# Performance work log

Hardware: AMD Instinct MI355X
Metric: run time of the kernel (lower is better)

## Reference

```python
import jax, jax.numpy as jnp
import numpy as np

# norse LIFParameters defaults
ALPHA = 100.0        # superspike surrogate slope
DT = 1e-3
TAU_SYN_INV = 200.0  # 1/5e-3
TAU_MEM_INV = 100.0  # 1/1e-2
V_TH = 1.0           # v_leak = v_reset = 0

@jax.custom_vjp
def heaviside(v):
    # forward: hard threshold; backward: superspike surrogate 1/(alpha*|v|+1)^2
    return (v > 0).astype(v.dtype)

def _hv_fwd(v):
    return heaviside(v), v

def _hv_bwd(v, g):
    return (g / (ALPHA * jnp.abs(v) + 1.0) ** 2,)

heaviside.defvjp(_hv_fwd, _hv_bwd)

def setup_inputs() -> dict:
    key = jax.random.key(0)
    ks = jax.random.split(key, 5)
    B, H, W, O = 2048, 15, 15, 10
    x = jax.random.uniform(ks[0], (B, 1, H, W), jnp.float32)  # image-like in [0,1)
    conv_w = jax.random.normal(ks[1], (2, 1, 4, 4), jnp.float32) * 0.25
    conv_b = jax.random.normal(ks[2], (2,), jnp.float32) * 0.1
    lin_w = jax.random.normal(ks[3], (O, 72), jnp.float32) * (1.0 / np.sqrt(72.0))
    lin_b = jax.random.normal(ks[4], (O,), jnp.float32) * 0.1
    return {"x": x, "conv_w": conv_w, "conv_b": conv_b,
            "lin_w": lin_w, "lin_b": lin_b, "num_steps": 300}

def reference(x, conv_w, conv_b, lin_w, lin_b, num_steps):
    B = x.shape[0]
    O = lin_w.shape[0]
    current = x * 10.0  # constant input current to the encoder

    def step(carry, _):
        v_enc, v, i = carry
        # --- constant_current_lif_encode step (lif_current_encoder) ---
        v_enc = v_enc + DT * TAU_MEM_INV * (-v_enc + current)
        z_in = heaviside(v_enc - V_TH)
        v_enc = v_enc - z_in * v_enc  # reset to v_reset = 0
        # --- feed-forward: conv -> maxpool(2) -> linear ---
        c = jax.lax.conv_general_dilated(
            z_in, conv_w, (1, 1), 'VALID',
            dimension_numbers=('NCHW', 'OIHW', 'NCHW')) + conv_b[None, :, None, None]
        p = jax.lax.reduce_window(c, -jnp.inf, jax.lax.max,
                                  (1, 1, 2, 2), (1, 1, 2, 2), 'VALID')  # [B,2,6,6]
        lin = p.reshape(B, -1) @ lin_w.T + lin_b  # [B,O]
        # --- norse LIFCell (lif_feed_forward_step) ---
        v_dec = v + DT * TAU_MEM_INV * (-v + i)
        i_dec = i - DT * TAU_SYN_INV * i
        spk = heaviside(v_dec - V_TH)
        v_new = (1.0 - spk) * v_dec  # v_reset = 0
        i_new = i_dec + lin
        return (v_enc, v_new, i_new), (spk, v_new)

    init = (jnp.zeros_like(current),
            jnp.zeros((B, O), x.dtype),
            jnp.zeros((B, O), x.dtype))
    _, (spk_rec, mem_rec) = jax.lax.scan(step, init, None, length=num_steps)
    spk_out = spk_rec.sum(0)  # [B,O]
    return spk_out, mem_rec, spk_rec
```

## Files before the change

### kernel.cpp

```cpp
#include <hip/hip_runtime.h>
#include <math.h>


typedef float v2f __attribute__((ext_vector_type(2)));

__global__ __launch_bounds__(128, 4) void snn_step_kernel(
    const float* __restrict__ x,
    const float* __restrict__ conv_w,
    const float* __restrict__ conv_b,
    const float* __restrict__ lin_w,
    const float* __restrict__ lin_b,
    float* __restrict__ out,
    int T, int B)
{
    const int b   = blockIdx.x;
    const int tid = threadIdx.x;
    const int w   = tid & 63;
    const int wv  = tid >> 6;

    __shared__ float  s_linw[720];
    __shared__ float  s_linb[10];
    __shared__ float4 s_lut[4][32];
    __shared__ unsigned int s_bits[2][16];
    __shared__ float  s_p[8][72];
    __shared__ float  s_part[64];

    for (int j = tid; j < 720; j += 128) s_linw[j] = lin_w[j];
    if (tid < 10) s_linb[tid] = lin_b[tid];
    {
        const int ky = tid >> 5, n = tid & 31;
        float s00 = 0.f, s01 = 0.f, s10 = 0.f, s11 = 0.f;
#pragma unroll
        for (int kx = 0; kx < 4; ++kx) {
            const float w0 = conv_w[ky * 4 + kx];
            const float w1 = conv_w[16 + ky * 4 + kx];
            if ((n >> kx) & 1)       { s00 += w0; s01 += w1; }
            if ((n >> (kx + 1)) & 1) { s10 += w0; s11 += w1; }
        }
        s_lut[ky][n] = make_float4(s00, s01, s10, s11);
    }
    __syncthreads();

    float ve[4], cur[4];
    v2f  cb2 = (v2f){0.f, 0.f};
    bool convlane = false;
    int  wordsel = 0, shx = 0, shx16 = 16;

    float lwreg[18];
    float lbias = 0.f;
    float v = 0.f, i_syn = 0.f, sc = 0.f;
    float svv[4], svs[4];
    const int lo = w >> 2, lq = w & 3;
    const size_t BO = (size_t)B * 10;
    float* mp  = out + BO + (size_t)b * 10 + w;
    float* spp = out + BO + (size_t)T * BO + (size_t)b * 10 + w;

    auto enc_pack = [&](int bufsel) {
        unsigned long long bal0, bal1, bal2, bal3;
        {
            float vn = __fadd_rn(ve[0], __fmul_rn(0.1f, __fsub_rn(cur[0], ve[0])));
            bool  sp = (vn > 1.0f);
            ve[0] = sp ? 0.f : vn;
            bal0  = __ballot(sp);
        }
        {
            float vn = __fadd_rn(ve[1], __fmul_rn(0.1f, __fsub_rn(cur[1], ve[1])));
            bool  sp = (vn > 1.0f);
            ve[1] = sp ? 0.f : vn;
            bal1  = __ballot(sp);
        }
        {
            float vn = __fadd_rn(ve[2], __fmul_rn(0.1f, __fsub_rn(cur[2], ve[2])));
            bool  sp = (vn > 1.0f);
            ve[2] = sp ? 0.f : vn;
            bal2  = __ballot(sp);
        }
        {
            float vn = __fadd_rn(ve[3], __fmul_rn(0.1f, __fsub_rn(cur[3], ve[3])));
            bool  sp = (vn > 1.0f);
            ve[3] = sp ? 0.f : vn;
            bal3  = __ballot(sp);
        }
        unsigned long long m01 = (w & 2) ? bal1 : bal0;
        unsigned long long m23 = (w & 2) ? bal3 : bal2;
        unsigned long long m   = (w & 4) ? m23 : m01;
        unsigned word = (unsigned)((w & 1) ? (m >> 32) : m);
        if (w < 8) s_bits[bufsel][w] = word;
    };

    if (wv == 0) {
        const int j   = w >> 4;
        const int col = w & 15;
#pragma unroll
        for (int k = 0; k < 4; ++k) {
            const int  row = 4 * k + j;
            const bool act = (col < 15) && (row < 15);
            ve[k]  = 0.f;
            cur[k] = act ? __fmul_rn(x[(size_t)b * 225 + row * 15 + col], 10.0f) : 0.f;
        }
        convlane = (w < 36);
        const int py = w / 6, px = w - 6 * py;
        wordsel = py;
        shx     = 2 * px;
        shx16   = shx + 16;
        cb2 = (v2f){conv_b[0], conv_b[1]};

        enc_pack(0);
    } else {
#pragma unroll
        for (int jj = 0; jj < 18; ++jj) {
            int idx = lo * 72 + lq * 18 + jj;
            lwreg[jj] = s_linw[idx < 720 ? idx : 719];
        }
        lbias = (w < 10) ? s_linb[w] : 0.f;
    }

    auto lin_comp = [&](const float* pbuf, int k) {
        const float* pp = &pbuf[lq * 18];
        float pv[18];
#pragma unroll
        for (int jj = 0; jj < 18; ++jj) pv[jj] = pp[jj];
        float partial = 0.0f;
#pragma unroll
        for (int jj = 0; jj < 18; ++jj)
            partial = fmaf(lwreg[jj], pv[jj], partial);
        s_part[w] = partial;

        float vd  = __fadd_rn(v, __fmul_rn(0.1f, __fsub_rn(i_syn, v)));
        float id  = __fsub_rn(i_syn, __fmul_rn(0.2f, i_syn));
        float spk = (vd > 1.0f) ? 1.0f : 0.0f;
        v = (vd > 1.0f) ? 0.0f : vd;
        sc += spk;
        svv[k] = v;
        svs[k] = spk;

        float4 pr = *(const float4*)&s_part[4 * (w < 10 ? w : 0)];
        float lin = __fadd_rn(__fadd_rn(__fadd_rn(__fadd_rn(pr.x, pr.y), pr.z), pr.w), lbias);
        i_syn = __fadd_rn(id, lin);
    };

    auto issue_stores = [&]() {
        if (w < 10) {
#pragma unroll
            for (int k = 0; k < 4; ++k) {
                mp[(size_t)k * BO]  = svv[k];
                spp[(size_t)k * BO] = svs[k];
            }
        }
        mp  += 4 * BO;
        spp += 4 * BO;
    };

    const int TI = T >> 2;

    for (int i = 0; i < TI; ++i) {
        if (wv == 0) {
#pragma unroll
            for (int k = 0; k < 4; ++k) {
                unsigned wb0 = 0, wb1 = 0, wb2 = 0;
                if (convlane) {
                    const unsigned* bb = &s_bits[k & 1][wordsel];
                    wb0 = bb[0]; wb1 = bb[1]; wb2 = bb[2];
                }

                enc_pack((k + 1) & 1);

                if (convlane) {
                    const int i0 = (wb0 >> shx)   & 31;
                    const int i1 = (wb0 >> shx16) & 31;
                    const int i2 = (wb1 >> shx)   & 31;
                    const int i3 = (wb1 >> shx16) & 31;
                    const int i4 = (wb2 >> shx)   & 31;

                    const float4 f0 = s_lut[0][i0];
                    const float4 f1 = s_lut[1][i1];
                    const float4 f2 = s_lut[2][i2];
                    const float4 f3 = s_lut[3][i3];
                    const float4 g0 = s_lut[0][i1];
                    const float4 g1 = s_lut[1][i2];
                    const float4 g2 = s_lut[2][i3];
                    const float4 g3 = s_lut[3][i4];

                    v2f a00 = (v2f){f0.x, f0.y};  a00 += (v2f){f1.x, f1.y};
                    a00 += (v2f){f2.x, f2.y};     a00 += (v2f){f3.x, f3.y};
                    v2f a01 = (v2f){f0.z, f0.w};  a01 += (v2f){f1.z, f1.w};
                    a01 += (v2f){f2.z, f2.w};     a01 += (v2f){f3.z, f3.w};
                    v2f a10 = (v2f){g0.x, g0.y};  a10 += (v2f){g1.x, g1.y};
                    a10 += (v2f){g2.x, g2.y};     a10 += (v2f){g3.x, g3.y};
                    v2f a11 = (v2f){g0.z, g0.w};  a11 += (v2f){g1.z, g1.w};
                    a11 += (v2f){g2.z, g2.w};     a11 += (v2f){g3.z, g3.w};

                    v2f v00 = a00 + cb2, v01 = a01 + cb2;
                    v2f v10 = a10 + cb2, v11 = a11 + cb2;
                    v2f m2 = __builtin_elementwise_max(
                                 __builtin_elementwise_max(v00, v01),
                                 __builtin_elementwise_max(v10, v11));

                    float* pbuf = s_p[((i & 1) << 2) | k];
                    pbuf[w]      = m2.x;
                    pbuf[36 + w] = m2.y;
                }
            }
        } else {
            if (i >= 2) issue_stores();
            if (i >= 1) {
#pragma unroll
                for (int k = 0; k < 4; ++k)
                    lin_comp(s_p[(((i - 1) & 1) << 2) | k], k);
            }
        }
        __syncthreads();
    }

    if (wv == 1) {
        issue_stores();
#pragma unroll
        for (int k = 0; k < 4; ++k)
            lin_comp(s_p[(((TI - 1) & 1) << 2) | k], k);
        issue_stores();
        if (w < 10) out[(size_t)b * 10 + w] = sc;
    }
}

extern "C" void kernel_launch(void* const* d_in, const int* in_sizes, int n_in,
                              void* d_out, int out_size, void* d_ws, size_t ws_size,
                              hipStream_t stream) {
    const float* x      = (const float*)d_in[0];
    const float* conv_w = (const float*)d_in[1];
    const float* conv_b = (const float*)d_in[2];
    const float* lin_w  = (const float*)d_in[3];
    const float* lin_b  = (const float*)d_in[4];
    float* out = (float*)d_out;

    const int B = in_sizes[0] / 225;
    const int T = (out_size / (B * 10) - 1) / 2;

    snn_step_kernel<<<B, 128, 0, stream>>>(x, conv_w, conv_b, lin_w, lin_b, out, T, B);
}
```

Before: 203.9 us.

## Merge producer and consumer waves into a single barrier-free wave

Collapses the two-wave block (encoder/conv wave and linear/LIF wave synchronized by __syncthreads) into one 64-lane wave that software-pipelines encode, conv and linear/LIF across consecutive timesteps. The pooled-feature buffer is repacked with padding so each quarter starts at a 20-float offset, and outputs are stored every step. This removes block barriers and cross-wave handoff, and halves threads per block so more blocks can be resident. In exchange the wave serializes all stage work and relies on intra-wave lockstep for shared-memory ordering.

```diff
diff --git a/kernel.cpp b/kernel.cpp
--- a/kernel.cpp
+++ b/kernel.cpp
@@ -4,7 +4,7 @@
 
 typedef float v2f __attribute__((ext_vector_type(2)));
 
-__global__ __launch_bounds__(128, 4) void snn_step_kernel(
+__global__ __launch_bounds__(64, 2) void snn_step_kernel(
     const float* __restrict__ x,
     const float* __restrict__ conv_w,
     const float* __restrict__ conv_b,
@@ -13,22 +13,22 @@
     float* __restrict__ out,
     int T, int B)
 {
-    const int b   = blockIdx.x;
-    const int tid = threadIdx.x;
-    const int w   = tid & 63;
-    const int wv  = tid >> 6;
+    const int b = blockIdx.x;
+    const int w = threadIdx.x;
 
     __shared__ float  s_linw[720];
     __shared__ float  s_linb[10];
     __shared__ float4 s_lut[4][32];
     __shared__ unsigned int s_bits[2][16];
-    __shared__ float  s_p[8][72];
+    __shared__ float  s_p[2][80];
     __shared__ float  s_part[64];
 
-    for (int j = tid; j < 720; j += 128) s_linw[j] = lin_w[j];
-    if (tid < 10) s_linb[tid] = lin_b[tid];
-    {
-        const int ky = tid >> 5, n = tid & 31;
+    for (int j = w; j < 720; j += 64) s_linw[j] = lin_w[j];
+    if (w < 10) s_linb[w] = lin_b[w];
+#pragma unroll
+    for (int e = 0; e < 2; ++e) {
+        const int t  = w + 64 * e;
+        const int ky = t >> 5, n = t & 31;
         float s00 = 0.f, s01 = 0.f, s10 = 0.f, s11 = 0.f;
 #pragma unroll
         for (int kx = 0; kx < 4; ++kx) {
@@ -41,16 +41,32 @@
     }
     __syncthreads();
 
+    const int jrow = w >> 4, col = w & 15;
     float ve[4], cur[4];
-    v2f  cb2 = (v2f){0.f, 0.f};
-    bool convlane = false;
-    int  wordsel = 0, shx = 0, shx16 = 16;
-
+#pragma unroll
+    for (int k = 0; k < 4; ++k) {
+        const int  row = 4 * k + jrow;
+        const bool act = (col < 15) && (row < 15);
+        ve[k]  = 0.f;
+        cur[k] = act ? __fmul_rn(x[(size_t)b * 225 + row * 15 + col], 10.0f) : 0.f;
+    }
+
+    const bool convlane = (w < 36);
+    const int py = w / 6, px = w - 6 * py;
+    const int wordsel = py;
+    const int shx = 2 * px, shx16 = shx + 16;
+    const int off0 = (w < 18) ? w : (w + 2);
+    const v2f cb2 = (v2f){conv_b[0], conv_b[1]};
+
+    const int lo = w >> 2, lq = w & 3;
     float lwreg[18];
-    float lbias = 0.f;
+#pragma unroll
+    for (int jj = 0; jj < 18; ++jj) {
+        int idx = lo * 72 + lq * 18 + jj;
+        lwreg[jj] = s_linw[idx < 720 ? idx : 719];
+    }
+    const float lbias = (w < 10) ? s_linb[w] : 0.f;
     float v = 0.f, i_syn = 0.f, sc = 0.f;
-    float svv[4], svs[4];
-    const int lo = w >> 2, lq = w & 3;
     const size_t BO = (size_t)B * 10;
     float* mp  = out + BO + (size_t)b * 10 + w;
     float* spp = out + BO + (size_t)T * BO + (size_t)b * 10 + w;
@@ -88,38 +104,74 @@
         if (w < 8) s_bits[bufsel][w] = word;
     };
 
-    if (wv == 0) {
-        const int j   = w >> 4;
-        const int col = w & 15;
-#pragma unroll
-        for (int k = 0; k < 4; ++k) {
-            const int  row = 4 * k + j;
-            const bool act = (col < 15) && (row < 15);
-            ve[k]  = 0.f;
-            cur[k] = act ? __fmul_rn(x[(size_t)b * 225 + row * 15 + col], 10.0f) : 0.f;
-        }
-        convlane = (w < 36);
-        const int py = w / 6, px = w - 6 * py;
-        wordsel = py;
-        shx     = 2 * px;
-        shx16   = shx + 16;
-        cb2 = (v2f){conv_b[0], conv_b[1]};
-
-        enc_pack(0);
-    } else {
-#pragma unroll
-        for (int jj = 0; jj < 18; ++jj) {
-            int idx = lo * 72 + lq * 18 + jj;
-            lwreg[jj] = s_linw[idx < 720 ? idx : 719];
-        }
-        lbias = (w < 10) ? s_linb[w] : 0.f;
-    }
-
-    auto lin_comp = [&](const float* pbuf, int k) {
-        const float* pp = &pbuf[lq * 18];
+    auto conv_lut = [&](unsigned wb0, unsigned wb1, unsigned wb2, int dbuf) {
+        const int i0 = (wb0 >> shx)   & 31;
+        const int i1 = (wb0 >> shx16) & 31;
+        const int i2 = (wb1 >> shx)   & 31;
+        const int i3 = (wb1 >> shx16) & 31;
+        const int i4 = (wb2 >> shx)   & 31;
+
+        const float4 f0 = s_lut[0][i0];
+        const float4 f1 = s_lut[1][i1];
+        const float4 f2 = s_lut[2][i2];
+        const float4 f3 = s_lut[3][i3];
+        const float4 g0 = s_lut[0][i1];
+        const float4 g1 = s_lut[1][i2];
+        const float4 g2 = s_lut[2][i3];
+        const float4 g3 = s_lut[3][i4];
+
+        v2f a00 = (v2f){f0.x, f0.y};  a00 += (v2f){f1.x, f1.y};
+        a00 += (v2f){f2.x, f2.y};     a00 += (v2f){f3.x, f3.y};
+        v2f a01 = (v2f){f0.z, f0.w};  a01 += (v2f){f1.z, f1.w};
+        a01 += (v2f){f2.z, f2.w};     a01 += (v2f){f3.z, f3.w};
+        v2f a10 = (v2f){g0.x, g0.y};  a10 += (v2f){g1.x, g1.y};
+        a10 += (v2f){g2.x, g2.y};     a10 += (v2f){g3.x, g3.y};
+        v2f a11 = (v2f){g0.z, g0.w};  a11 += (v2f){g1.z, g1.w};
+        a11 += (v2f){g2.z, g2.w};     a11 += (v2f){g3.z, g3.w};
+
+        v2f v00 = a00 + cb2, v01 = a01 + cb2;
+        v2f v10 = a10 + cb2, v11 = a11 + cb2;
+        v2f m2 = __builtin_elementwise_max(
+                     __builtin_elementwise_max(v00, v01),
+                     __builtin_elementwise_max(v10, v11));
+
+        float* pbuf = s_p[dbuf];
+        pbuf[off0]      = m2.x;
+        pbuf[off0 + 40] = m2.y;
+    };
+
+    enc_pack(0);
+    enc_pack(1);
+    {
+        unsigned wb0 = 0, wb1 = 0, wb2 = 0;
+        if (convlane) {
+            const unsigned* bb = &s_bits[0][wordsel];
+            wb0 = bb[0]; wb1 = bb[1]; wb2 = bb[2];
+        }
+        if (convlane) conv_lut(wb0, wb1, wb2, 0);
+    }
+
+    for (int i = 0; i < T; ++i) {
+        const int pb = i & 1;
+        const int cb = pb ^ 1;
+
+        unsigned wb0 = 0, wb1 = 0, wb2 = 0;
+        if (convlane) {
+            const unsigned* bb = &s_bits[cb][wordsel];
+            wb0 = bb[0]; wb1 = bb[1]; wb2 = bb[2];
+        }
+
         float pv[18];
-#pragma unroll
-        for (int jj = 0; jj < 18; ++jj) pv[jj] = pp[jj];
+        {
+            const float* pp = &s_p[pb][lq * 20];
+#pragma unroll
+            for (int jj = 0; jj < 18; ++jj) pv[jj] = pp[jj];
+        }
+
+        enc_pack(pb);
+
+        if (convlane) conv_lut(wb0, wb1, wb2, cb);
+
         float partial = 0.0f;
 #pragma unroll
         for (int jj = 0; jj < 18; ++jj)
@@ -131,95 +183,17 @@
         float spk = (vd > 1.0f) ? 1.0f : 0.0f;
         v = (vd > 1.0f) ? 0.0f : vd;
         sc += spk;
-        svv[k] = v;
-        svs[k] = spk;
 
         float4 pr = *(const float4*)&s_part[4 * (w < 10 ? w : 0)];
         float lin = __fadd_rn(__fadd_rn(__fadd_rn(__fadd_rn(pr.x, pr.y), pr.z), pr.w), lbias);
         i_syn = __fadd_rn(id, lin);
-    };
-
-    auto issue_stores = [&]() {
-        if (w < 10) {
-#pragma unroll
-            for (int k = 0; k < 4; ++k) {
-                mp[(size_t)k * BO]  = svv[k];
-                spp[(size_t)k * BO] = svs[k];
-            }
-        }
-        mp  += 4 * BO;
-        spp += 4 * BO;
-    };
-
-    const int TI = T >> 2;
-
-    for (int i = 0; i < TI; ++i) {
-        if (wv == 0) {
-#pragma unroll
-            for (int k = 0; k < 4; ++k) {
-                unsigned wb0 = 0, wb1 = 0, wb2 = 0;
-                if (convlane) {
-                    const unsigned* bb = &s_bits[k & 1][wordsel];
-                    wb0 = bb[0]; wb1 = bb[1]; wb2 = bb[2];
-                }
-
-                enc_pack((k + 1) & 1);
-
-                if (convlane) {
-                    const int i0 = (wb0 >> shx)   & 31;
-                    const int i1 = (wb0 >> shx16) & 31;
-                    const int i2 = (wb1 >> shx)   & 31;
-                    const int i3 = (wb1 >> shx16) & 31;
-                    const int i4 = (wb2 >> shx)   & 31;
-
-                    const float4 f0 = s_lut[0][i0];
-                    const float4 f1 = s_lut[1][i1];
-                    const float4 f2 = s_lut[2][i2];
-                    const float4 f3 = s_lut[3][i3];
-                    const float4 g0 = s_lut[0][i1];
-                    const float4 g1 = s_lut[1][i2];
-                    const float4 g2 = s_lut[2][i3];
-                    const float4 g3 = s_lut[3][i4];
-
-                    v2f a00 = (v2f){f0.x, f0.y};  a00 += (v2f){f1.x, f1.y};
-                    a00 += (v2f){f2.x, f2.y};     a00 += (v2f){f3.x, f3.y};
-                    v2f a01 = (v2f){f0.z, f0.w};  a01 += (v2f){f1.z, f1.w};
-                    a01 += (v2f){f2.z, f2.w};     a01 += (v2f){f3.z, f3.w};
-                    v2f a10 = (v2f){g0.x, g0.y};  a10 += (v2f){g1.x, g1.y};
-                    a10 += (v2f){g2.x, g2.y};     a10 += (v2f){g3.x, g3.y};
-                    v2f a11 = (v2f){g0.z, g0.w};  a11 += (v2f){g1.z, g1.w};
-                    a11 += (v2f){g2.z, g2.w};     a11 += (v2f){g3.z, g3.w};
-
-                    v2f v00 = a00 + cb2, v01 = a01 + cb2;
-                    v2f v10 = a10 + cb2, v11 = a11 + cb2;
-                    v2f m2 = __builtin_elementwise_max(
-                                 __builtin_elementwise_max(v00, v01),
-                                 __builtin_elementwise_max(v10, v11));
-
-                    float* pbuf = s_p[((i & 1) << 2) | k];
-                    pbuf[w]      = m2.x;
-                    pbuf[36 + w] = m2.y;
-                }
-            }
-        } else {
-            if (i >= 2) issue_stores();
-            if (i >= 1) {
-#pragma unroll
-                for (int k = 0; k < 4; ++k)
-                    lin_comp(s_p[(((i - 1) & 1) << 2) | k], k);
-            }
-        }
-        __syncthreads();
-    }
-
-    if (wv == 1) {
-        issue_stores();
-#pragma unroll
-        for (int k = 0; k < 4; ++k)
-            lin_comp(s_p[(((TI - 1) & 1) << 2) | k], k);
-        issue_stores();
-        if (w < 10) out[(size_t)b * 10 + w] = sc;
-    }
+
+        if (w < 10) { *mp = v; *spp = spk; }
+        mp  += BO;
+        spp += BO;
+    }
+
+    if (w < 10) out[(size_t)b * 10 + w] = sc;
 }
 
 extern "C" void kernel_launch(void* const* d_in, const int* in_sizes, int n_in,
@@ -235,5 +209,5 @@
     const int B = in_sizes[0] / 225;
     const int T = (out_size / (B * 10) - 1) / 2;
 
-    snn_step_kernel<<<B, 128, 0, stream>>>(x, conv_w, conv_b, lin_w, lin_b, out, T, B);
+    snn_step_kernel<<<B, 64, 0, stream>>>(x, conv_w, conv_b, lin_w, lin_b, out, T, B);
 }
```

After: 212.7 us. +4.3%, slower.

## Split pipeline across three waves: encoder/decoder wave and two conv+linear waves

Applied to the files above, without the earlier changes.

Moves from a two-wave pipeline to three waves per block. One wave handles encoding and the LIF decode, and two waves share the conv+pool+linear work by alternating timesteps. An 8-slot spike-bit ring and a per-step linear-result buffer let these stages run in parallel. The role-to-wave mapping is rotated per block, presumably to spread load across SIMDs. This shortens the critical per-group work but raises threads per block and the number of pipeline stages, which lengthens prologue and epilogue and may lower occupancy.

```diff
diff --git a/kernel.cpp b/kernel.cpp
--- a/kernel.cpp
+++ b/kernel.cpp
@@ -4,7 +4,7 @@
 
 typedef float v2f __attribute__((ext_vector_type(2)));
 
-__global__ __launch_bounds__(128, 4) void snn_step_kernel(
+__global__ __launch_bounds__(192, 6) void snn_step_kernel(
     const float* __restrict__ x,
     const float* __restrict__ conv_w,
     const float* __restrict__ conv_b,
@@ -13,21 +13,23 @@
     float* __restrict__ out,
     int T, int B)
 {
-    const int b   = blockIdx.x;
-    const int tid = threadIdx.x;
-    const int w   = tid & 63;
-    const int wv  = tid >> 6;
-
-    __shared__ float  s_linw[720];
-    __shared__ float  s_linb[10];
-    __shared__ float4 s_lut[4][32];
-    __shared__ unsigned int s_bits[2][16];
-    __shared__ float  s_p[8][72];
-    __shared__ float  s_part[64];
-
-    for (int j = tid; j < 720; j += 128) s_linw[j] = lin_w[j];
+    const int b    = blockIdx.x;
+    const int tid  = threadIdx.x;
+    const int w    = tid & 63;
+    const int wv   = tid >> 6;
+    const int role = (wv + b) % 3;
+
+    __shared__ float    s_linw[720];
+    __shared__ float    s_linb[10];
+    __shared__ float4   s_lut[4][32];
+    __shared__ unsigned s_bits[8][16];
+    __shared__ float    s_lin[8][12];
+    __shared__ float    s_p[2][80];
+    __shared__ float    s_part[2][64];
+
+    for (int j = tid; j < 720; j += 192) s_linw[j] = lin_w[j];
     if (tid < 10) s_linb[tid] = lin_b[tid];
-    {
+    if (tid < 128) {
         const int ky = tid >> 5, n = tid & 31;
         float s00 = 0.f, s01 = 0.f, s10 = 0.f, s11 = 0.f;
 #pragma unroll
@@ -42,20 +44,39 @@
     __syncthreads();
 
     float ve[4], cur[4];
-    v2f  cb2 = (v2f){0.f, 0.f};
-    bool convlane = false;
-    int  wordsel = 0, shx = 0, shx16 = 16;
-
-    float lwreg[18];
-    float lbias = 0.f;
     float v = 0.f, i_syn = 0.f, sc = 0.f;
     float svv[4], svs[4];
-    const int lo = w >> 2, lq = w & 3;
     const size_t BO = (size_t)B * 10;
     float* mp  = out + BO + (size_t)b * 10 + w;
     float* spp = out + BO + (size_t)T * BO + (size_t)b * 10 + w;
-
-    auto enc_pack = [&](int bufsel) {
+    {
+        const int jrow = w >> 4, col = w & 15;
+#pragma unroll
+        for (int k = 0; k < 4; ++k) {
+            const int  row = 4 * k + jrow;
+            const bool act = (col < 15) && (row < 15) && (role == 0);
+            ve[k]  = 0.f;
+            cur[k] = act ? __fmul_rn(x[(size_t)b * 225 + row * 15 + col], 10.0f) : 0.f;
+        }
+    }
+
+    const int  r1 = (role == 2) ? 1 : 0;
+    const bool convlane = (w < 36);
+    const int  py = w / 6, px = w - 6 * py;
+    const int  wordsel = py;
+    const int  shx = 2 * px, shx16 = shx + 16;
+    const int  off0 = (w < 18) ? w : (w + 2);
+    const v2f  cb2 = (v2f){conv_b[0], conv_b[1]};
+    const int  lo = w >> 2, lq = w & 3;
+    float lwreg[18];
+#pragma unroll
+    for (int jj = 0; jj < 18; ++jj) {
+        int idx = lo * 72 + lq * 18 + jj;
+        lwreg[jj] = s_linw[idx < 720 ? idx : 719];
+    }
+    const float lbias = (w < 10) ? s_linb[w] : 0.f;
+
+    auto enc_pack = [&](int slot) {
         unsigned long long bal0, bal1, bal2, bal3;
         {
             float vn = __fadd_rn(ve[0], __fmul_rn(0.1f, __fsub_rn(cur[0], ve[0])));
@@ -85,47 +106,72 @@
         unsigned long long m23 = (w & 2) ? bal3 : bal2;
         unsigned long long m   = (w & 4) ? m23 : m01;
         unsigned word = (unsigned)((w & 1) ? (m >> 32) : m);
-        if (w < 8) s_bits[bufsel][w] = word;
-    };
-
-    if (wv == 0) {
-        const int j   = w >> 4;
-        const int col = w & 15;
-#pragma unroll
-        for (int k = 0; k < 4; ++k) {
-            const int  row = 4 * k + j;
-            const bool act = (col < 15) && (row < 15);
-            ve[k]  = 0.f;
-            cur[k] = act ? __fmul_rn(x[(size_t)b * 225 + row * 15 + col], 10.0f) : 0.f;
-        }
-        convlane = (w < 36);
-        const int py = w / 6, px = w - 6 * py;
-        wordsel = py;
-        shx     = 2 * px;
-        shx16   = shx + 16;
-        cb2 = (v2f){conv_b[0], conv_b[1]};
-
-        enc_pack(0);
-    } else {
-#pragma unroll
-        for (int jj = 0; jj < 18; ++jj) {
-            int idx = lo * 72 + lq * 18 + jj;
-            lwreg[jj] = s_linw[idx < 720 ? idx : 719];
-        }
-        lbias = (w < 10) ? s_linb[w] : 0.f;
-    }
-
-    auto lin_comp = [&](const float* pbuf, int k) {
-        const float* pp = &pbuf[lq * 18];
+        if (w < 8) s_bits[slot][w] = word;
+    };
+
+    auto conv_lin = [&](int t) {
+        const int slot = t & 7;
+        if (convlane) {
+            const unsigned* bb = &s_bits[slot][wordsel];
+            const unsigned wb0 = bb[0], wb1 = bb[1], wb2 = bb[2];
+
+            const int i0 = (wb0 >> shx)   & 31;
+            const int i1 = (wb0 >> shx16) & 31;
+            const int i2 = (wb1 >> shx)   & 31;
+            const int i3 = (wb1 >> shx16) & 31;
+            const int i4 = (wb2 >> shx)   & 31;
+
+            const float4 f0 = s_lut[0][i0];
+            const float4 f1 = s_lut[1][i1];
+            const float4 f2 = s_lut[2][i2];
+            const float4 f3 = s_lut[3][i3];
+            const float4 g0 = s_lut[0][i1];
+            const float4 g1 = s_lut[1][i2];
+            const float4 g2 = s_lut[2][i3];
+            const float4 g3 = s_lut[3][i4];
+
+            v2f a00 = (v2f){f0.x, f0.y};  a00 += (v2f){f1.x, f1.y};
+            a00 += (v2f){f2.x, f2.y};     a00 += (v2f){f3.x, f3.y};
+            v2f a01 = (v2f){f0.z, f0.w};  a01 += (v2f){f1.z, f1.w};
+            a01 += (v2f){f2.z, f2.w};     a01 += (v2f){f3.z, f3.w};
+            v2f a10 = (v2f){g0.x, g0.y};  a10 += (v2f){g1.x, g1.y};
+            a10 += (v2f){g2.x, g2.y};     a10 += (v2f){g3.x, g3.y};
+            v2f a11 = (v2f){g0.z, g0.w};  a11 += (v2f){g1.z, g1.w};
+            a11 += (v2f){g2.z, g2.w};     a11 += (v2f){g3.z, g3.w};
+
+            v2f v00 = a00 + cb2, v01 = a01 + cb2;
+            v2f v10 = a10 + cb2, v11 = a11 + cb2;
+            v2f m2 = __builtin_elementwise_max(
+                         __builtin_elementwise_max(v00, v01),
+                         __builtin_elementwise_max(v10, v11));
+
+            float* pbuf = s_p[r1];
+            pbuf[off0]      = m2.x;
+            pbuf[off0 + 40] = m2.y;
+        }
+        asm volatile("" ::: "memory");
+
         float pv[18];
-#pragma unroll
-        for (int jj = 0; jj < 18; ++jj) pv[jj] = pp[jj];
+        {
+            const float* pp = &s_p[r1][lq * 20];
+#pragma unroll
+            for (int jj = 0; jj < 18; ++jj) pv[jj] = pp[jj];
+        }
         float partial = 0.0f;
 #pragma unroll
         for (int jj = 0; jj < 18; ++jj)
             partial = fmaf(lwreg[jj], pv[jj], partial);
-        s_part[w] = partial;
-
+        s_part[r1][w] = partial;
+        asm volatile("" ::: "memory");
+
+        float4 pr = *(const float4*)&s_part[r1][4 * (w < 10 ? w : 0)];
+        float lin = __fadd_rn(__fadd_rn(__fadd_rn(__fadd_rn(pr.x, pr.y), pr.z), pr.w), lbias);
+        if (w < 10) s_lin[slot][w] = lin;
+    };
+
+    const int li = (w < 10) ? w : 10;
+    auto dec_step = [&](int t, int k) {
+        float lv  = s_lin[t & 7][li];
         float vd  = __fadd_rn(v, __fmul_rn(0.1f, __fsub_rn(i_syn, v)));
         float id  = __fsub_rn(i_syn, __fmul_rn(0.2f, i_syn));
         float spk = (vd > 1.0f) ? 1.0f : 0.0f;
@@ -133,10 +179,7 @@
         sc += spk;
         svv[k] = v;
         svs[k] = spk;
-
-        float4 pr = *(const float4*)&s_part[4 * (w < 10 ? w : 0)];
-        float lin = __fadd_rn(__fadd_rn(__fadd_rn(__fadd_rn(pr.x, pr.y), pr.z), pr.w), lbias);
-        i_syn = __fadd_rn(id, lin);
+        i_syn = __fadd_rn(id, lv);
     };
 
     auto issue_stores = [&]() {
@@ -151,72 +194,44 @@
         spp += 4 * BO;
     };
 
-    const int TI = T >> 2;
-
-    for (int i = 0; i < TI; ++i) {
-        if (wv == 0) {
-#pragma unroll
-            for (int k = 0; k < 4; ++k) {
-                unsigned wb0 = 0, wb1 = 0, wb2 = 0;
-                if (convlane) {
-                    const unsigned* bb = &s_bits[k & 1][wordsel];
-                    wb0 = bb[0]; wb1 = bb[1]; wb2 = bb[2];
-                }
-
-                enc_pack((k + 1) & 1);
-
-                if (convlane) {
-                    const int i0 = (wb0 >> shx)   & 31;
-                    const int i1 = (wb0 >> shx16) & 31;
-                    const int i2 = (wb1 >> shx)   & 31;
-                    const int i3 = (wb1 >> shx16) & 31;
-                    const int i4 = (wb2 >> shx)   & 31;
-
-                    const float4 f0 = s_lut[0][i0];
-                    const float4 f1 = s_lut[1][i1];
-                    const float4 f2 = s_lut[2][i2];
-                    const float4 f3 = s_lut[3][i3];
-                    const float4 g0 = s_lut[0][i1];
-                    const float4 g1 = s_lut[1][i2];
-                    const float4 g2 = s_lut[2][i3];
-                    const float4 g3 = s_lut[3][i4];
-
-                    v2f a00 = (v2f){f0.x, f0.y};  a00 += (v2f){f1.x, f1.y};
-                    a00 += (v2f){f2.x, f2.y};     a00 += (v2f){f3.x, f3.y};
-                    v2f a01 = (v2f){f0.z, f0.w};  a01 += (v2f){f1.z, f1.w};
-                    a01 += (v2f){f2.z, f2.w};     a01 += (v2f){f3.z, f3.w};
-                    v2f a10 = (v2f){g0.x, g0.y};  a10 += (v2f){g1.x, g1.y};
-                    a10 += (v2f){g2.x, g2.y};     a10 += (v2f){g3.x, g3.y};
-                    v2f a11 = (v2f){g0.z, g0.w};  a11 += (v2f){g1.z, g1.w};
-                    a11 += (v2f){g2.z, g2.w};     a11 += (v2f){g3.z, g3.w};
-
-                    v2f v00 = a00 + cb2, v01 = a01 + cb2;
-                    v2f v10 = a10 + cb2, v11 = a11 + cb2;
-                    v2f m2 = __builtin_elementwise_max(
-                                 __builtin_elementwise_max(v00, v01),
-                                 __builtin_elementwise_max(v10, v11));
-
-                    float* pbuf = s_p[((i & 1) << 2) | k];
-                    pbuf[w]      = m2.x;
-                    pbuf[36 + w] = m2.y;
-                }
+    const int NG = T >> 2;
+
+    for (int g = 0; g < NG; ++g) {
+        const int base = 4 * g;
+        if (role == 0) {
+            if (g >= 3) issue_stores();
+#pragma unroll
+            for (int k = 0; k < 4; ++k)
+                enc_pack((base + k) & 7);
+            if (g >= 2) {
+#pragma unroll
+                for (int k = 0; k < 4; ++k)
+                    dec_step(base - 8 + k, k);
             }
         } else {
-            if (i >= 2) issue_stores();
-            if (i >= 1) {
-#pragma unroll
-                for (int k = 0; k < 4; ++k)
-                    lin_comp(s_p[(((i - 1) & 1) << 2) | k], k);
+            if (g >= 1) {
+                for (int k = role - 1; k < 4; k += 2)
+                    conv_lin(base - 4 + k);
             }
         }
         __syncthreads();
     }
 
-    if (wv == 1) {
+    if (role != 0) {
+        for (int k = role - 1; k < 4; k += 2)
+            conv_lin(T - 4 + k);
+    } else {
         issue_stores();
 #pragma unroll
         for (int k = 0; k < 4; ++k)
-            lin_comp(s_p[(((TI - 1) & 1) << 2) | k], k);
+            dec_step(T - 8 + k, k);
+    }
+    __syncthreads();
+    if (role == 0) {
+        issue_stores();
+#pragma unroll
+        for (int k = 0; k < 4; ++k)
+            dec_step(T - 4 + k, k);
         issue_stores();
         if (w < 10) out[(size_t)b * 10 + w] = sc;
     }
@@ -235,5 +250,5 @@
     const int B = in_sizes[0] / 225;
     const int T = (out_size / (B * 10) - 1) / 2;
 
-    snn_step_kernel<<<B, 128, 0, stream>>>(x, conv_w, conv_b, lin_w, lin_b, out, T, B);
+    snn_step_kernel<<<B, 192, 0, stream>>>(x, conv_w, conv_b, lin_w, lin_b, out, T, B);
 }
```

Measured after the change: 256.7 us. +25.9%, slower.

## Rebalance warp pipeline: 6-step groups, split conv across waves, shuffle reductions

Applied to the files above, without the earlier changes.

Each barrier interval now covers 6 timesteps instead of 4, and the spike bitmasks and pooled buffers become 16-slot rings. Wave 0 encodes 6 steps and convolves 4 of them, while wave 1 convolves the remaining 2 before running the linear and LIF updates. The linear partial-sum reduction uses xor shuffles in place of an LDS round trip, which removes the s_part scratch buffer. The aim is to balance work between the two waves and reduce barriers per step, at the cost of more LDS and registers and an assumption that T is divisible by 6.

```diff
diff --git a/kernel.cpp b/kernel.cpp
--- a/kernel.cpp
+++ b/kernel.cpp
@@ -18,12 +18,11 @@
     const int w   = tid & 63;
     const int wv  = tid >> 6;
 
-    __shared__ float  s_linw[720];
-    __shared__ float  s_linb[10];
-    __shared__ float4 s_lut[4][32];
-    __shared__ unsigned int s_bits[2][16];
-    __shared__ float  s_p[8][72];
-    __shared__ float  s_part[64];
+    __shared__ float    s_linw[720];
+    __shared__ float    s_linb[10];
+    __shared__ float4   s_lut[4][32];
+    __shared__ unsigned s_bits[16][8];
+    __shared__ float    s_p[16][80];
 
     for (int j = tid; j < 720; j += 128) s_linw[j] = lin_w[j];
     if (tid < 10) s_linb[tid] = lin_b[tid];
@@ -42,20 +41,39 @@
     __syncthreads();
 
     float ve[4], cur[4];
-    v2f  cb2 = (v2f){0.f, 0.f};
-    bool convlane = false;
-    int  wordsel = 0, shx = 0, shx16 = 16;
-
+    {
+        const int jrow = w >> 4, col = w & 15;
+#pragma unroll
+        for (int k = 0; k < 4; ++k) {
+            const int  row = 4 * k + jrow;
+            const bool act = (col < 15) && (row < 15) && (wv == 0);
+            ve[k]  = 0.f;
+            cur[k] = act ? __fmul_rn(x[(size_t)b * 225 + row * 15 + col], 10.0f) : 0.f;
+        }
+    }
+
+    const bool convlane = (w < 36);
+    const int  py = w / 6, px = w - 6 * py;
+    const int  wordsel = py;
+    const int  shx = 2 * px, shx16 = shx + 16;
+    const int  off0 = (w < 18) ? w : (w + 2);
+    const v2f  cb2 = (v2f){conv_b[0], conv_b[1]};
+
+    const int lo = w >> 2, lq = w & 3;
     float lwreg[18];
-    float lbias = 0.f;
+#pragma unroll
+    for (int jj = 0; jj < 18; ++jj) {
+        int idx = lo * 72 + lq * 18 + jj;
+        lwreg[jj] = s_linw[idx < 720 ? idx : 719];
+    }
+    const float lbias = s_linb[lo < 10 ? lo : 0];
     float v = 0.f, i_syn = 0.f, sc = 0.f;
-    float svv[4], svs[4];
-    const int lo = w >> 2, lq = w & 3;
+    float svv[6], svs[6];
     const size_t BO = (size_t)B * 10;
-    float* mp  = out + BO + (size_t)b * 10 + w;
-    float* spp = out + BO + (size_t)T * BO + (size_t)b * 10 + w;
-
-    auto enc_pack = [&](int bufsel) {
+    float* mp  = out + BO + (size_t)b * 10 + lo;
+    float* spp = out + BO + (size_t)T * BO + (size_t)b * 10 + lo;
+
+    auto enc_pack = [&](int slot) {
         unsigned long long bal0, bal1, bal2, bal3;
         {
             float vn = __fadd_rn(ve[0], __fmul_rn(0.1f, __fsub_rn(cur[0], ve[0])));
@@ -85,38 +103,47 @@
         unsigned long long m23 = (w & 2) ? bal3 : bal2;
         unsigned long long m   = (w & 4) ? m23 : m01;
         unsigned word = (unsigned)((w & 1) ? (m >> 32) : m);
-        if (w < 8) s_bits[bufsel][w] = word;
-    };
-
-    if (wv == 0) {
-        const int j   = w >> 4;
-        const int col = w & 15;
-#pragma unroll
-        for (int k = 0; k < 4; ++k) {
-            const int  row = 4 * k + j;
-            const bool act = (col < 15) && (row < 15);
-            ve[k]  = 0.f;
-            cur[k] = act ? __fmul_rn(x[(size_t)b * 225 + row * 15 + col], 10.0f) : 0.f;
-        }
-        convlane = (w < 36);
-        const int py = w / 6, px = w - 6 * py;
-        wordsel = py;
-        shx     = 2 * px;
-        shx16   = shx + 16;
-        cb2 = (v2f){conv_b[0], conv_b[1]};
-
-        enc_pack(0);
-    } else {
-#pragma unroll
-        for (int jj = 0; jj < 18; ++jj) {
-            int idx = lo * 72 + lq * 18 + jj;
-            lwreg[jj] = s_linw[idx < 720 ? idx : 719];
-        }
-        lbias = (w < 10) ? s_linb[w] : 0.f;
-    }
-
-    auto lin_comp = [&](const float* pbuf, int k) {
-        const float* pp = &pbuf[lq * 18];
+        if (w < 8) s_bits[slot][w] = word;
+    };
+
+    auto conv_compute = [&](int slot, unsigned wb0, unsigned wb1, unsigned wb2) {
+        const int i0 = (wb0 >> shx)   & 31;
+        const int i1 = (wb0 >> shx16) & 31;
+        const int i2 = (wb1 >> shx)   & 31;
+        const int i3 = (wb1 >> shx16) & 31;
+        const int i4 = (wb2 >> shx)   & 31;
+
+        const float4 f0 = s_lut[0][i0];
+        const float4 f1 = s_lut[1][i1];
+        const float4 f2 = s_lut[2][i2];
+        const float4 f3 = s_lut[3][i3];
+        const float4 g0 = s_lut[0][i1];
+        const float4 g1 = s_lut[1][i2];
+        const float4 g2 = s_lut[2][i3];
+        const float4 g3 = s_lut[3][i4];
+
+        v2f a00 = (v2f){f0.x, f0.y};  a00 += (v2f){f1.x, f1.y};
+        a00 += (v2f){f2.x, f2.y};     a00 += (v2f){f3.x, f3.y};
+        v2f a01 = (v2f){f0.z, f0.w};  a01 += (v2f){f1.z, f1.w};
+        a01 += (v2f){f2.z, f2.w};     a01 += (v2f){f3.z, f3.w};
+        v2f a10 = (v2f){g0.x, g0.y};  a10 += (v2f){g1.x, g1.y};
+        a10 += (v2f){g2.x, g2.y};     a10 += (v2f){g3.x, g3.y};
+        v2f a11 = (v2f){g0.z, g0.w};  a11 += (v2f){g1.z, g1.w};
+        a11 += (v2f){g2.z, g2.w};     a11 += (v2f){g3.z, g3.w};
+
+        v2f v00 = a00 + cb2, v01 = a01 + cb2;
+        v2f v10 = a10 + cb2, v11 = a11 + cb2;
+        v2f m2 = __builtin_elementwise_max(
+                     __builtin_elementwise_max(v00, v01),
+                     __builtin_elementwise_max(v10, v11));
+
+        float* pbuf = s_p[slot];
+        pbuf[off0]      = m2.x;
+        pbuf[off0 + 40] = m2.y;
+    };
+
+    auto lin_dec = [&](int s, int k) {
+        const float* pp = &s_p[s & 15][lq * 20];
         float pv[18];
 #pragma unroll
         for (int jj = 0; jj < 18; ++jj) pv[jj] = pp[jj];
@@ -124,7 +151,12 @@
 #pragma unroll
         for (int jj = 0; jj < 18; ++jj)
             partial = fmaf(lwreg[jj], pv[jj], partial);
-        s_part[w] = partial;
+
+        float p1 = __shfl_xor(partial, 1);
+        float p2 = __shfl_xor(partial, 2);
+        float p3 = __shfl_xor(partial, 3);
+        float lin = __fadd_rn(
+            __fadd_rn(__fadd_rn(__fadd_rn(partial, p1), p2), p3), lbias);
 
         float vd  = __fadd_rn(v, __fmul_rn(0.1f, __fsub_rn(i_syn, v)));
         float id  = __fsub_rn(i_syn, __fmul_rn(0.2f, i_syn));
@@ -133,80 +165,57 @@
         sc += spk;
         svv[k] = v;
         svs[k] = spk;
-
-        float4 pr = *(const float4*)&s_part[4 * (w < 10 ? w : 0)];
-        float lin = __fadd_rn(__fadd_rn(__fadd_rn(__fadd_rn(pr.x, pr.y), pr.z), pr.w), lbias);
         i_syn = __fadd_rn(id, lin);
     };
 
     auto issue_stores = [&]() {
-        if (w < 10) {
-#pragma unroll
-            for (int k = 0; k < 4; ++k) {
+        if (lq == 0 && lo < 10) {
+#pragma unroll
+            for (int k = 0; k < 6; ++k) {
                 mp[(size_t)k * BO]  = svv[k];
                 spp[(size_t)k * BO] = svs[k];
             }
         }
-        mp  += 4 * BO;
-        spp += 4 * BO;
-    };
-
-    const int TI = T >> 2;
-
-    for (int i = 0; i < TI; ++i) {
+        mp  += 6 * BO;
+        spp += 6 * BO;
+    };
+
+    if (wv == 0) enc_pack(0);
+
+    const int NG = T / 6;
+
+    for (int g = 0; g < NG; ++g) {
+        const int base = 6 * g;
         if (wv == 0) {
 #pragma unroll
             for (int k = 0; k < 4; ++k) {
+                const int s = base + k;
                 unsigned wb0 = 0, wb1 = 0, wb2 = 0;
                 if (convlane) {
-                    const unsigned* bb = &s_bits[k & 1][wordsel];
+                    const unsigned* bb = &s_bits[s & 15][wordsel];
                     wb0 = bb[0]; wb1 = bb[1]; wb2 = bb[2];
                 }
-
-                enc_pack((k + 1) & 1);
-
+                enc_pack((s + 1) & 15);
+                if (convlane) conv_compute(s & 15, wb0, wb1, wb2);
+            }
+            enc_pack((base + 5) & 15);
+            enc_pack((base + 6) & 15);
+        } else {
+            if (g >= 2) issue_stores();
+            if (g >= 1) {
+                const int pb = base - 6;
+                unsigned a0 = 0, a1 = 0, a2 = 0, c0 = 0, c1 = 0, c2 = 0;
                 if (convlane) {
-                    const int i0 = (wb0 >> shx)   & 31;
-                    const int i1 = (wb0 >> shx16) & 31;
-                    const int i2 = (wb1 >> shx)   & 31;
-                    const int i3 = (wb1 >> shx16) & 31;
-                    const int i4 = (wb2 >> shx)   & 31;
-
-                    const float4 f0 = s_lut[0][i0];
-                    const float4 f1 = s_lut[1][i1];
-                    const float4 f2 = s_lut[2][i2];
-                    const float4 f3 = s_lut[3][i3];
-                    const float4 g0 = s_lut[0][i1];
-                    const float4 g1 = s_lut[1][i2];
-                    const float4 g2 = s_lut[2][i3];
-                    const float4 g3 = s_lut[3][i4];
-
-                    v2f a00 = (v2f){f0.x, f0.y};  a00 += (v2f){f1.x, f1.y};
-                    a00 += (v2f){f2.x, f2.y};     a00 += (v2f){f3.x, f3.y};
-                    v2f a01 = (v2f){f0.z, f0.w};  a01 += (v2f){f1.z, f1.w};
-                    a01 += (v2f){f2.z, f2.w};     a01 += (v2f){f3.z, f3.w};
-                    v2f a10 = (v2f){g0.x, g0.y};  a10 += (v2f){g1.x, g1.y};
-                    a10 += (v2f){g2.x, g2.y};     a10 += (v2f){g3.x, g3.y};
-                    v2f a11 = (v2f){g0.z, g0.w};  a11 += (v2f){g1.z, g1.w};
-                    a11 += (v2f){g2.z, g2.w};     a11 += (v2f){g3.z, g3.w};
-
-                    v2f v00 = a00 + cb2, v01 = a01 + cb2;
-                    v2f v10 = a10 + cb2, v11 = a11 + cb2;
-                    v2f m2 = __builtin_elementwise_max(
-                                 __builtin_elementwise_max(v00, v01),
-                                 __builtin_elementwise_max(v10, v11));
-
-                    float* pbuf = s_p[((i & 1) << 2) | k];
-                    pbuf[w]      = m2.x;
-                    pbuf[36 + w] = m2.y;
+                    const unsigned* ba = &s_bits[(pb + 4) & 15][wordsel];
+                    a0 = ba[0]; a1 = ba[1]; a2 = ba[2];
+                    const unsigned* bc = &s_bits[(pb + 5) & 15][wordsel];
+                    c0 = bc[0]; c1 = bc[1]; c2 = bc[2];
+                    conv_compute((pb + 4) & 15, a0, a1, a2);
+                    conv_compute((pb + 5) & 15, c0, c1, c2);
                 }
-            }
-        } else {
-            if (i >= 2) issue_stores();
-            if (i >= 1) {
-#pragma unroll
-                for (int k = 0; k < 4; ++k)
-                    lin_comp(s_p[(((i - 1) & 1) << 2) | k], k);
+#pragma unroll
+                for (int k = 0; k < 6; ++k)
+                    lin_dec(pb + k, k);
             }
         }
         __syncthreads();
@@ -214,11 +223,21 @@
 
     if (wv == 1) {
         issue_stores();
-#pragma unroll
-        for (int k = 0; k < 4; ++k)
-            lin_comp(s_p[(((TI - 1) & 1) << 2) | k], k);
+        const int pb = 6 * (NG - 1);
+        unsigned a0 = 0, a1 = 0, a2 = 0, c0 = 0, c1 = 0, c2 = 0;
+        if (convlane) {
+            const unsigned* ba = &s_bits[(pb + 4) & 15][wordsel];
+            a0 = ba[0]; a1 = ba[1]; a2 = ba[2];
+            const unsigned* bc = &s_bits[(pb + 5) & 15][wordsel];
+            c0 = bc[0]; c1 = bc[1]; c2 = bc[2];
+            conv_compute((pb + 4) & 15, a0, a1, a2);
+            conv_compute((pb + 5) & 15, c0, c1, c2);
+        }
+#pragma unroll
+        for (int k = 0; k < 6; ++k)
+            lin_dec(pb + k, k);
         issue_stores();
-        if (w < 10) out[(size_t)b * 10 + w] = sc;
+        if (lq == 0 && lo < 10) out[(size_t)b * 10 + lo] = sc;
     }
 }
 
```

Measured after the change: 198.3 us. 1.03x faster.
